# Performance work log

Hardware: AMD Instinct MI355X
Metric: run time of the kernel (lower is better)

Reference implementation:

```python
import jax, jax.numpy as jnp
import numpy as np


def setup_inputs() -> dict:
    key = jax.random.key(0)
    k1, k2 = jax.random.split(key)
    x = jax.random.normal(k1, (2, 320, 4, 32, 32), dtype=jnp.float32)
    W = jax.random.uniform(k2, (640, 1), dtype=jnp.float32)  # torch.rand init
    return {"x": x, "W": W}


def reference(x, W):
    # x: [B, C, D, H, W_], W: [2C, 1]
    B, C, D, H, W_ = x.shape
    N = D * H * W_
    p = x.reshape(B, C, N)  # proj_temp
    w1 = W[:C, 0]   # multiplies temp[k] (the varying row of temp_b)
    w2 = W[C:, 0]   # multiplies temp[j] (the broadcast row)
    s1 = jnp.einsum('bcn,c->bn', p, w1)  # per-position score for column index k
    s2 = jnp.einsum('bcn,c->bn', p, w2)  # per-position score for row index j
    # energy[b, j, k] = w1 . x_k + w2 . x_j  (additive outer-sum decomposition)
    energy = s1[:, None, :] + s2[:, :, None]  # [B, N, N]
    attention = jax.nn.softmax(jax.nn.leaky_relu(energy, negative_slope=0.01), axis=-1)
    # out = bmm(p, attention^T): out[b,c,n] = sum_k p[b,c,k] * attention[b,n,k]
    out = jnp.einsum('bck,bnk->bcn', p, attention) + p
    return out.reshape(B, C, D, H, W_)
```

## Files before the change

### kernel.cpp

```cpp
#include <hip/hip_runtime.h>
#include <hip/hip_bf16.h>

#define C_DIM 320
#define N_DIM 4096
#define NEG 0.01f

typedef float f32x4 __attribute__((ext_vector_type(4)));
typedef float f32x2 __attribute__((ext_vector_type(2)));
typedef short bf16x8 __attribute__((ext_vector_type(8)));
typedef __bf16 bfv8 __attribute__((ext_vector_type(8)));

__device__ __forceinline__ float lrelu(float e) { return fmaxf(e, NEG * e); }

__device__ __forceinline__ unsigned short bf16bits(float v) {
    __hip_bfloat16 h = __float2bfloat16(v);
    return *(unsigned short*)&h;
}
__device__ __forceinline__ float bf16tof(unsigned short u) {
    unsigned int bits = ((unsigned int)u) << 16;
    return __builtin_bit_cast(float, bits);
}

__device__ __forceinline__ void gload_lds16(const void* g, void* l) {
    __builtin_amdgcn_global_load_lds(
        (const __attribute__((address_space(1))) void*)g,
        (__attribute__((address_space(3))) void*)l, 16, 0, 0);
}

__device__ __forceinline__ float fold5(const float* __restrict__ p, int b, int i) {
    float v = p[((size_t)(b * 5 + 0)) * N_DIM + i];
    v += p[((size_t)(b * 5 + 1)) * N_DIM + i];
    v += p[((size_t)(b * 5 + 2)) * N_DIM + i];
    v += p[((size_t)(b * 5 + 3)) * N_DIM + i];
    v += p[((size_t)(b * 5 + 4)) * N_DIM + i];
    return v;
}


__global__ __launch_bounds__(256) void k_pre(const float* __restrict__ x,
                                             const float* __restrict__ W,
                                             float* __restrict__ s1p,
                                             float* __restrict__ s2p,
                                             short* __restrict__ xT) {
    __shared__ float tile[64][65];
    __shared__ float r1[4][64], r2[4][64];
    const int b = blockIdx.z, cg = blockIdx.y, nb = blockIdx.x;
    const int nl = threadIdx.x & 63, cw = threadIdx.x >> 6;
    const int n0 = nb * 64, c0 = cg * 64;
    const int n = n0 + nl;
    float a1 = 0.f, a2 = 0.f;
    #pragma unroll
    for (int cc = 0; cc < 16; ++cc) {
        const int cl = cw * 16 + cc;
        const int c = c0 + cl;
        float v = x[((size_t)(b * C_DIM + c)) * N_DIM + n];
        a1 = fmaf(v, W[c], a1);
        a2 = fmaf(v, W[C_DIM + c], a2);
        tile[cl][nl] = v;
    }
    r1[cw][nl] = a1; r2[cw][nl] = a2;
    __syncthreads();
    const int half = nl >> 5;
    const int cp = nl & 31;
    #pragma unroll
    for (int rr = 0; rr < 8; ++rr) {
        const int nr = cw * 16 + rr * 2 + half;
        unsigned int pk = (unsigned int)bf16bits(tile[2 * cp][nr])
                        | ((unsigned int)bf16bits(tile[2 * cp + 1][nr]) << 16);
        *(unsigned int*)&xT[((size_t)b * N_DIM + n0 + nr) * C_DIM + c0 + 2 * cp] = pk;
    }
    if (threadIdx.x < 64) {
        float t1 = r1[0][nl] + r1[1][nl] + r1[2][nl] + r1[3][nl];
        float t2 = r2[0][nl] + r2[1][nl] + r2[2][nl] + r2[3][nl];
        s1p[((size_t)(b * 5 + cg)) * N_DIM + n] = t1;
        s2p[((size_t)(b * 5 + cg)) * N_DIM + n] = t2;
    }
}

__global__ __launch_bounds__(256) void k_rank(const float* __restrict__ s1p,
                                              int* __restrict__ pcnt) {
    __shared__ float ch[512];
    const int chunk = blockIdx.x, kt = blockIdx.y, b = blockIdx.z;
    const int tid = threadIdx.x;
    const int kbase = chunk * 512;
    ch[tid] = fold5(s1p, b, kbase + tid);
    ch[tid + 256] = fold5(s1p, b, kbase + tid + 256);
    __syncthreads();
    const int k = kt * 256 + tid;
    const float v = fold5(s1p, b, k);
    int cnt = 0;
    #pragma unroll 8
    for (int i = 0; i < 512; ++i) {
        float sv = ch[i];
        int kc = kbase + i;
        cnt += (sv < v || (sv == v && kc < k)) ? 1 : 0;
    }
    pcnt[(b * 8 + chunk) * N_DIM + k] = cnt;
}

__global__ __launch_bounds__(1024) void k_sct(const float* __restrict__ s1p,
                                              const int* __restrict__ pcnt,
                                              float* __restrict__ Sg,
                                              int* __restrict__ idxg,
                                              float* __restrict__ EP,
                                              float* __restrict__ GP,
                                              float* __restrict__ Eg,
                                              float* __restrict__ Gg) {
    __shared__ float sv[4096];
    __shared__ int si[4096];
    __shared__ float wte[16], wtg[16];
    const int b = blockIdx.x, tid = threadIdx.x;
    #pragma unroll
    for (int q = 0; q < 4; ++q) {
        const int k = q * 1024 + tid;
        int r = 0;
        #pragma unroll
        for (int c = 0; c < 8; ++c) r += pcnt[(b * 8 + c) * N_DIM + k];
        sv[r] = fold5(s1p, b, k);
        si[r] = k;
    }
    __syncthreads();
    const int j0 = tid * 4;
    float pe[4], pg[4];
    {
        float v0 = sv[j0], v1 = sv[j0 + 1], v2 = sv[j0 + 2], v3 = sv[j0 + 3];
        float e0 = __expf(v0), e1 = __expf(v1), e2 = __expf(v2), e3 = __expf(v3);
        float g0 = __expf(NEG * v0), g1 = __expf(NEG * v1);
        float g2 = __expf(NEG * v2), g3 = __expf(NEG * v3);
        Eg[b * N_DIM + j0] = e0; Eg[b * N_DIM + j0 + 1] = e1;
        Eg[b * N_DIM + j0 + 2] = e2; Eg[b * N_DIM + j0 + 3] = e3;
        Gg[b * N_DIM + j0] = g0; Gg[b * N_DIM + j0 + 1] = g1;
        Gg[b * N_DIM + j0 + 2] = g2; Gg[b * N_DIM + j0 + 3] = g3;
        pe[0] = e0; pe[1] = pe[0] + e1; pe[2] = pe[1] + e2; pe[3] = pe[2] + e3;
        pg[0] = g0; pg[1] = pg[0] + g1; pg[2] = pg[1] + g2; pg[3] = pg[2] + g3;
    }
    const float te = pe[3], tg = pg[3];
    const int lane = tid & 63, wid = tid >> 6;
    float ie = te, ig = tg;
    #pragma unroll
    for (int o = 1; o < 64; o <<= 1) {
        float ue = __shfl_up(ie, o);
        float ug = __shfl_up(ig, o);
        if (lane >= o) { ie += ue; ig += ug; }
    }
    if (lane == 63) { wte[wid] = ie; wtg[wid] = ig; }
    __syncthreads();
    float oe = 0.f, og = 0.f;
    for (int wq = 0; wq < wid; ++wq) { oe += wte[wq]; og += wtg[wq]; }
    const float be = oe + ie - te, bg = og + ig - tg;
    #pragma unroll
    for (int i = 0; i < 4; ++i) {
        EP[b * 4097 + j0 + i] = be + (i ? pe[i - 1] : 0.f);
        GP[b * 4097 + j0 + i] = bg + (i ? pg[i - 1] : 0.f);
    }
    if (tid == 1023) {
        EP[b * 4097 + 4096] = oe + ie;
        GP[b * 4097 + 4096] = og + ig;
    }
    #pragma unroll
    for (int q = 0; q < 4; ++q) {
        const int j = q * 1024 + tid;
        Sg[b * N_DIM + j] = sv[j];
        idxg[b * N_DIM + j] = si[j];
    }
}

__global__ __launch_bounds__(256) void k_pjz(const short* __restrict__ xT,
                                             const int* __restrict__ idxg,
                                             const float* __restrict__ Eg,
                                             const float* __restrict__ Gg,
                                             const float* __restrict__ Sg,
                                             const float* __restrict__ EP,
                                             const float* __restrict__ GP,
                                             const float* __restrict__ s2p,
                                             unsigned int* __restrict__ Tloc,
                                             float* __restrict__ tot,
                                             int* __restrict__ JnA,
                                             float* __restrict__ fzA,
                                             float* __restrict__ hzA) {
    __shared__ float Sl[4096];
    const int w = threadIdx.x >> 6, l = threadIdx.x & 63;
    const int bx = blockIdx.x;
    if (bx < 160) {
        const int jt4 = bx & 15;
        const int cg = (bx >> 4) % 5;
        const int b = bx / 80;
        const int tile = jt4 * 4 + w;
        const int jbase = tile * 64;
        const int c = cg * 64 + l;
        const short* xTb = xT + (size_t)b * N_DIM * C_DIM;
        const float ej = Eg[b * N_DIM + jbase + l];
        const float gj = Gg[b * N_DIM + jbase + l];
        const int   ij = idxg[b * N_DIM + jbase + l];
        unsigned short xv[64];
        #pragma unroll
        for (int j = 0; j < 64; ++j) {
            const int kidx = __shfl(ij, j);
            xv[j] = (unsigned short)xTb[(size_t)kidx * C_DIM + c];
        }
        float se = 0.f, sg = 0.f;
        #pragma unroll
        for (int j = 0; j < 64; ++j) {
            const float e = __shfl(ej, j);
            const float g = __shfl(gj, j);
            const float x0 = bf16tof(xv[j]);
            se = fmaf(x0, e, se);
            sg = fmaf(x0, g, sg);
            Tloc[((size_t)b * N_DIM + jbase + j) * C_DIM + c] =
                (unsigned int)bf16bits(se) | ((unsigned int)bf16bits(sg) << 16);
        }
        *(f32x2*)&tot[(((size_t)b * 64 + tile) * C_DIM + c) * 2] = (f32x2){se, sg};
    } else {
        const int jb = bx - 160;
        const int b = jb >> 4;
        const int nbase = (jb & 15) * 256;
        for (int i = threadIdx.x; i < 4096; i += 256) Sl[i] = Sg[b * N_DIM + i];
        __syncthreads();
        const float smax = Sl[4095];
        const float EPt = EP[b * 4097 + 4096];
        const int n = nbase + threadIdx.x;
        const float s2n = fold5(s2p, b, n);
        const float mn = lrelu(s2n + smax);
        const float F = __expf(s2n - mn), H = __expf(NEG * s2n - mn);
        const float t = -s2n;
        int lo = 0, hi = 4096;
        while (lo < hi) {
            int mid = (lo + hi) >> 1;
            if (Sl[mid] < t) lo = mid + 1; else hi = mid;
        }
        const float suf = EPt - EP[b * 4097 + lo];
        const float pre = GP[b * 4097 + lo];
        const float rz = 1.f / (F * suf + H * pre);
        JnA[b * N_DIM + n] = lo;
        fzA[b * N_DIM + n] = F * rz;
        hzA[b * N_DIM + n] = H * rz;
    }
}

__global__ __launch_bounds__(256) void k_out(const float* __restrict__ x,
                                             const unsigned int* __restrict__ Tloc,
                                             const float* __restrict__ tot,
                                             const int* __restrict__ JnA,
                                             const float* __restrict__ fzA,
                                             const float* __restrict__ hzA,
                                             float* __restrict__ out) {
    __shared__ float offl[65][64][2];
    __shared__ float wsum[4][64][2];
    __shared__ float tile[64][65];
    const int b = blockIdx.z, cg = blockIdx.y, n0 = blockIdx.x * 64;
    const int tid = threadIdx.x, w = tid >> 6, l = tid & 63;
    const int c0 = cg * 64;

    float ae = 0.f, ag = 0.f;
    #pragma unroll
    for (int i = 0; i < 16; ++i) {
        const int jt = w * 16 + i;
        offl[jt][l][0] = ae; offl[jt][l][1] = ag;
        f32x2 v = *(const f32x2*)&tot[(((size_t)b * 64 + jt) * C_DIM + c0 + l) * 2];
        ae += v[0]; ag += v[1];
    }
    wsum[w][l][0] = ae; wsum[w][l][1] = ag;
    __syncthreads();
    float be = 0.f, bg = 0.f;
    for (int ww = 0; ww < w; ++ww) { be += wsum[ww][l][0]; bg += wsum[ww][l][1]; }
    #pragma unroll
    for (int i = 0; i < 16; ++i) {
        const int jt = w * 16 + i;
        offl[jt][l][0] += be; offl[jt][l][1] += bg;
    }
    if (w == 3) { offl[64][l][0] = be + ae; offl[64][l][1] = bg + ag; }
    __syncthreads();

    const float gtE = offl[64][l][0];

    #pragma unroll
    for (int half = 0; half < 2; ++half) {
        unsigned int tvp[8];
        f32x2 ov[8];
        float fzs[8], hzs[8], msk[8];
        #pragma unroll
        for (int i = 0; i < 8; ++i) {
            const int n = n0 + w * 16 + half * 8 + i;
            const int Jn = JnA[b * N_DIM + n];
            fzs[i] = fzA[b * N_DIM + n];
            hzs[i] = hzA[b * N_DIM + n];
            const int jt = Jn >> 6, jl = Jn & 63;
            msk[i] = jl ? 1.f : 0.f;
            const int jrow = jl ? (Jn - 1) : 0;
            ov[i][0] = offl[jt][l][0];
            ov[i][1] = offl[jt][l][1];
            tvp[i] = Tloc[((size_t)b * N_DIM + jrow) * C_DIM + c0 + l];
        }
        #pragma unroll
        for (int i = 0; i < 8; ++i) {
            const float tvE = bf16tof((unsigned short)(tvp[i] & 0xFFFFu));
            const float tvG = bf16tof((unsigned short)(tvp[i] >> 16));
            const float se_ex = ov[i][0] + msk[i] * tvE;
            const float sg_ex = ov[i][1] + msk[i] * tvG;
            tile[l][w * 16 + half * 8 + i] = fzs[i] * (gtE - se_ex) + hzs[i] * sg_ex;
        }
    }
    __syncthreads();
    const int row = tid >> 2, nseg = (tid & 3) * 16;
    const size_t gidx = ((size_t)(b * C_DIM + c0 + row)) * N_DIM + n0 + nseg;
    #pragma unroll
    for (int i2 = 0; i2 < 16; i2 += 4) {
        f32x4 xv = *(const f32x4*)&x[gidx + i2];
        f32x4 o;
        #pragma unroll
        for (int q = 0; q < 4; ++q) o[q] = tile[row][nseg + i2 + q] + xv[q];
        *(f32x4*)&out[gidx + i2] = o;
    }
}


__global__ __launch_bounds__(256) void k_s12(const float* __restrict__ x,
                                             const float* __restrict__ W,
                                             float* __restrict__ s1p,
                                             float* __restrict__ s2p,
                                             short* __restrict__ xb) {
    const int b = blockIdx.z, cb = blockIdx.y;
    const int nl = threadIdx.x & 63, cw = threadIdx.x >> 6;
    const int n = blockIdx.x * 64 + nl;
    const int cbase = cb * 64 + cw * 16;
    const float* px = x + ((size_t)b * C_DIM + cbase) * N_DIM + n;
    short* pxb = xb + ((size_t)b * C_DIM + cbase) * N_DIM + n;
    const float* w1 = W + cbase;
    const float* w2 = W + C_DIM + cbase;
    float a1 = 0.f, a2 = 0.f;
    #pragma unroll
    for (int cc = 0; cc < 16; ++cc) {
        float v = px[(size_t)cc * N_DIM];
        a1 = fmaf(v, w1[cc], a1);
        a2 = fmaf(v, w2[cc], a2);
        __hip_bfloat16 hv = __float2bfloat16(v);
        pxb[(size_t)cc * N_DIM] = *(short*)&hv;
    }
    __shared__ float r1[4][64], r2[4][64];
    r1[cw][nl] = a1; r2[cw][nl] = a2;
    __syncthreads();
    if (threadIdx.x < 64) {
        s1p[((size_t)b * 5 + cb) * N_DIM + n] = r1[0][nl] + r1[1][nl] + r1[2][nl] + r1[3][nl];
        s2p[((size_t)b * 5 + cb) * N_DIM + n] = r2[0][nl] + r2[1][nl] + r2[2][nl] + r2[3][nl];
    }
}

__global__ __launch_bounds__(1024) void k_fold(const float* __restrict__ s1p,
                                               const float* __restrict__ s2p,
                                               float* __restrict__ s2,
                                               float* __restrict__ Ekf,
                                               float* __restrict__ Gkf,
                                               float* __restrict__ s1max) {
    const int b = blockIdx.x, tid = threadIdx.x;
    __shared__ float md[1024];
    float mx = -3.4e38f;
    for (int n = tid; n < N_DIM; n += 1024) {
        float v1 = 0.f, v2 = 0.f;
        #pragma unroll
        for (int cb = 0; cb < 5; ++cb) {
            v1 += s1p[((size_t)b * 5 + cb) * N_DIM + n];
            v2 += s2p[((size_t)b * 5 + cb) * N_DIM + n];
        }
        s2[b * N_DIM + n] = v2;
        Ekf[b * N_DIM + n] = __expf(v1);
        Gkf[b * N_DIM + n] = __expf(NEG * v1);
        mx = fmaxf(mx, v1);
    }
    md[tid] = mx;
    __syncthreads();
    for (int s = 512; s > 0; s >>= 1) {
        if (tid < s) md[tid] = fmaxf(md[tid], md[tid + s]);
        __syncthreads();
    }
    if (tid == 0) s1max[b] = md[0];
}

__global__ __launch_bounds__(256) void k_z(const float* __restrict__ s2,
                                           const float* __restrict__ s1max,
                                           const float* __restrict__ Ekf,
                                           const float* __restrict__ Gkf,
                                           float* __restrict__ Fz,
                                           float* __restrict__ Hz) {
    __shared__ __align__(16) float Els[4096], Gls[4096];
    const int b = blockIdx.y, tid = threadIdx.x;
    const int w = tid >> 6, l = tid & 63;
    const float* Eb = Ekf + b * N_DIM;
    const float* Gb = Gkf + b * N_DIM;
    #pragma unroll
    for (int i = 0; i < 4; ++i) {
        int chn = i * 256 + tid;
        *(f32x4*)&Els[chn * 4] = *(const f32x4*)&Eb[chn * 4];
        *(f32x4*)&Gls[chn * 4] = *(const f32x4*)&Gb[chn * 4];
    }
    __syncthreads();
    float smax = s1max[b];
    #pragma unroll
    for (int rr = 0; rr < 4; ++rr) {
        int row = b * N_DIM + blockIdx.x * 16 + w * 4 + rr;
        float s2n = s2[row];
        float mn = lrelu(s2n + smax);
        float F = __expf(s2n - mn), H = __expf(NEG * s2n - mn);
        float sum = 0.f;
        #pragma unroll 4
        for (int i = 0; i < 16; ++i) {
            int k = i * 256 + l * 4;
            f32x4 e = *(const f32x4*)&Els[k];
            f32x4 gg = *(const f32x4*)&Gls[k];
            #pragma unroll
            for (int j = 0; j < 4; ++j) sum += fmaxf(e[j] * F, gg[j] * H);
        }
        #pragma unroll
        for (int off = 32; off > 0; off >>= 1) sum += __shfl_down(sum, off);
        if (l == 0) {
            float rz = 1.f / sum;
            Fz[row] = F * rz;
            Hz[row] = H * rz;
        }
    }
}

__global__ __launch_bounds__(128) void k_gemm(const short* __restrict__ xb,
                                              const float* __restrict__ x,
                                              const float* __restrict__ Ekf,
                                              const float* __restrict__ Gkf,
                                              const float* __restrict__ Fz,
                                              const float* __restrict__ Hz,
                                              float* __restrict__ out) {
    __shared__ __align__(16) short Asm[2][2][4096];
    __shared__ __align__(16) float EGs[2][2][256];

    const int b = blockIdx.z, c0 = blockIdx.y * 64, n0 = blockIdx.x * 64;
    const int tid = threadIdx.x;
    const int h = tid >> 6, l = tid & 63, lr = l & 15, g = l >> 4;
    const short* xbp = xb + (size_t)b * C_DIM * N_DIM + h * 2048;
    const float* Eb = Ekf + b * N_DIM + h * 2048;
    const float* Gb = Gkf + b * N_DIM + h * 2048;

    int ncol[4]; float fz[4], hz[4];
    #pragma unroll
    for (int t = 0; t < 4; ++t) {
        int n = n0 + t * 16 + lr;
        ncol[t] = n;
        fz[t] = Fz[b * N_DIM + n];
        hz[t] = Hz[b * N_DIM + n];
    }

    f32x4 acc[4][4];
    #pragma unroll
    for (int i = 0; i < 4; ++i)
        #pragma unroll
        for (int t = 0; t < 4; ++t) acc[i][t] = (f32x4){0.f, 0.f, 0.f, 0.f};

    auto stageA = [&](int buf, int it) {
        #pragma unroll
        for (int i = 0; i < 8; ++i) {
            int row = i * 8 + (l >> 3);
            int c8 = (l & 7) ^ (row & 7);
            gload_lds16(xbp + (size_t)(c0 + row) * N_DIM + it * 64 + c8 * 8,
                        &Asm[h][buf][i * 512]);
        }
    };
    auto stageEG = [&](int buf, int it) {
        int lm = l & 31;
        const float* p = (lm < 16) ? (Eb + it * 64 + lm * 4)
                                   : (Gb + it * 64 + (lm - 16) * 4);
        gload_lds16(p, &EGs[h][buf][0]);
    };

    stageA(0, 0); stageEG(0, 0);
    for (int it = 0; it < 32; ++it) {
        const int buf = it & 1;
        if (it < 31) {
            stageA(buf ^ 1, it + 1);
            stageEG(buf ^ 1, it + 1);
            asm volatile("s_waitcnt vmcnt(9)" ::: "memory");
        } else {
            asm volatile("s_waitcnt vmcnt(0)" ::: "memory");
        }
        __builtin_amdgcn_sched_barrier(0);
        #pragma unroll
        for (int s = 0; s < 2; ++s) {
            const int kk = s * 32 + g * 8;
            f32x4 e0 = *(const f32x4*)&EGs[h][buf][kk];
            f32x4 e1 = *(const f32x4*)&EGs[h][buf][kk + 4];
            f32x4 g0 = *(const f32x4*)&EGs[h][buf][64 + kk];
            f32x4 g1 = *(const f32x4*)&EGs[h][buf][64 + kk + 4];
            bf16x8 afr[4];
            #pragma unroll
            for (int i = 0; i < 4; ++i) {
                int row = 16 * i + lr;
                int idx = row * 64 + (((4 * s + g) ^ (row & 7)) * 8);
                afr[i] = *(const bf16x8*)&Asm[h][buf][idx];
            }
            bf16x8 bfr[4];
            #pragma unroll
            for (int t = 0; t < 4; ++t) {
                bfv8 qv;
                #pragma unroll
                for (int j = 0; j < 4; ++j) {
                    qv[j]     = (__bf16)fmaxf(e0[j] * fz[t], g0[j] * hz[t]);
                    qv[j + 4] = (__bf16)fmaxf(e1[j] * fz[t], g1[j] * hz[t]);
                }
                bfr[t] = __builtin_bit_cast(bf16x8, qv);
            }
            #pragma unroll
            for (int i = 0; i < 4; ++i)
                #pragma unroll
                for (int t = 0; t < 4; ++t)
                    acc[i][t] = __builtin_amdgcn_mfma_f32_16x16x32_bf16(
                        afr[i], bfr[t], acc[i][t], 0, 0, 0);
        }
    }

    __syncthreads();
    float* red = (float*)&Asm[0][0][0];
    if (h == 1) {
        #pragma unroll
        for (int i = 0; i < 4; ++i)
            #pragma unroll
            for (int t = 0; t < 4; ++t)
                #pragma unroll
                for (int r = 0; r < 4; ++r)
                    red[((i * 4 + t) * 4 + r) * 64 + l] = acc[i][t][r];
    }
    __syncthreads();
    if (h == 0) {
        #pragma unroll
        for (int i = 0; i < 4; ++i)
            #pragma unroll
            for (int t = 0; t < 4; ++t)
                #pragma unroll
                for (int r = 0; r < 4; ++r) {
                    float v = acc[i][t][r] + red[((i * 4 + t) * 4 + r) * 64 + l];
                    int c = c0 + 16 * i + g * 4 + r;
                    size_t idx = ((size_t)(b * C_DIM + c)) * N_DIM + ncol[t];
                    out[idx] = v + x[idx];
                }
    }
}


extern "C" void kernel_launch(void* const* d_in, const int* in_sizes, int n_in,
                              void* d_out, int out_size, void* d_ws, size_t ws_size,
                              hipStream_t stream) {
    const float* x = (const float*)d_in[0];
    const float* W = (const float*)d_in[1];
    float* out = (float*)d_out;
    float* ws = (float*)d_ws;

    const size_t o_s1p = 0,
                 o_s2p = 40960,
                 o_S   = 81920,
                 o_idx = 90112,
                 o_Eg  = 98304,
                 o_Gg  = 106496,
                 o_EP  = 114688,
                 o_GP  = 122882,
                 o_Jn  = 131076,
                 o_fz  = 139268,
                 o_hz  = 147460,
                 o_pc  = 155652,
                 o_tot = 221188,
                 o_xT  = 303108,
                 o_Tl  = 1613828,
                 o_end = 4235268;
    const size_t need_new = o_end * 4;

    const size_t m_s1p = 0, m_s2p = 40960, m_s2 = 81920, m_Ek = 90112,
                 m_Gk = 98304, m_Fz = 106496, m_Hz = 114688, m_mx = 122880,
                 m_xb = 122888;
    const size_t need_mid = m_xb * 4 + (size_t)2 * C_DIM * N_DIM * 2;

    if (ws_size >= need_new) {
        float* s1p = ws + o_s1p;
        float* s2p = ws + o_s2p;
        float* Sg = ws + o_S;
        int*   idxg = (int*)(ws + o_idx);
        float* Eg = ws + o_Eg;
        float* Gg = ws + o_Gg;
        float* EP = ws + o_EP;
        float* GP = ws + o_GP;
        int*   JnA = (int*)(ws + o_Jn);
        float* fzA = ws + o_fz;
        float* hzA = ws + o_hz;
        int*   pcnt = (int*)(ws + o_pc);
        float* tot = ws + o_tot;
        short* xT = (short*)(ws + o_xT);
        unsigned int* Tloc = (unsigned int*)(ws + o_Tl);

        k_pre <<<dim3(64, 5, 2), 256, 0, stream>>>(x, W, s1p, s2p, xT);
        k_rank<<<dim3(8, 16, 2), 256, 0, stream>>>(s1p, pcnt);
        k_sct <<<2, 1024, 0, stream>>>(s1p, pcnt, Sg, idxg, EP, GP, Eg, Gg);
        k_pjz <<<192, 256, 0, stream>>>(xT, idxg, Eg, Gg, Sg, EP, GP, s2p,
                                        Tloc, tot, JnA, fzA, hzA);
        k_out <<<dim3(64, 5, 2), 256, 0, stream>>>(x, Tloc, tot, JnA, fzA, hzA, out);
    } else {
        float* s1p = ws + m_s1p;
        float* s2p = ws + m_s2p;
        float* s2  = ws + m_s2;
        float* Ekf = ws + m_Ek;
        float* Gkf = ws + m_Gk;
        float* Fz  = ws + m_Fz;
        float* Hz  = ws + m_Hz;
        float* s1max = ws + m_mx;
        short* xb = (short*)(ws + m_xb);
        k_s12 <<<dim3(64, 5, 2), 256, 0, stream>>>(x, W, s1p, s2p, xb);
        k_fold<<<2, 1024, 0, stream>>>(s1p, s2p, s2, Ekf, Gkf, s1max);
        k_z   <<<dim3(256, 2), 256, 0, stream>>>(s2, s1max, Ekf, Gkf, Fz, Hz);
        k_gemm<<<dim3(64, 5, 2), 128, 0, stream>>>(xb, x, Ekf, Gkf, Fz, Hz, out);
    }
}
```

Before: 48.42 us.

## Parallelize scatter kernel and move prefix scan into z-computation blocks

The scatter kernel, previously two 1024-thread blocks that also computed prefix sums, becomes a 32-block grid. Each thread writes its sorted value, index and exponentials directly to the slot given by its rank. The exclusive prefix sums of E and G are now recomputed inside each of the 32 z-computing blocks of k_pjz, using shared-memory scans. This spreads a serial, two-block step across more CUs and removes the EP/GP global round trip. In exchange the scan work is repeated per block and k_pjz uses more shared memory (about 48 KB).

```diff
diff --git a/kernel.cpp b/kernel.cpp
--- a/kernel.cpp
+++ b/kernel.cpp
@@ -98,71 +98,22 @@
     pcnt[(b * 8 + chunk) * N_DIM + k] = cnt;
 }
 
-__global__ __launch_bounds__(1024) void k_sct(const float* __restrict__ s1p,
-                                              const int* __restrict__ pcnt,
-                                              float* __restrict__ Sg,
-                                              int* __restrict__ idxg,
-                                              float* __restrict__ EP,
-                                              float* __restrict__ GP,
-                                              float* __restrict__ Eg,
-                                              float* __restrict__ Gg) {
-    __shared__ float sv[4096];
-    __shared__ int si[4096];
-    __shared__ float wte[16], wtg[16];
-    const int b = blockIdx.x, tid = threadIdx.x;
-    #pragma unroll
-    for (int q = 0; q < 4; ++q) {
-        const int k = q * 1024 + tid;
-        int r = 0;
-        #pragma unroll
-        for (int c = 0; c < 8; ++c) r += pcnt[(b * 8 + c) * N_DIM + k];
-        sv[r] = fold5(s1p, b, k);
-        si[r] = k;
-    }
-    __syncthreads();
-    const int j0 = tid * 4;
-    float pe[4], pg[4];
-    {
-        float v0 = sv[j0], v1 = sv[j0 + 1], v2 = sv[j0 + 2], v3 = sv[j0 + 3];
-        float e0 = __expf(v0), e1 = __expf(v1), e2 = __expf(v2), e3 = __expf(v3);
-        float g0 = __expf(NEG * v0), g1 = __expf(NEG * v1);
-        float g2 = __expf(NEG * v2), g3 = __expf(NEG * v3);
-        Eg[b * N_DIM + j0] = e0; Eg[b * N_DIM + j0 + 1] = e1;
-        Eg[b * N_DIM + j0 + 2] = e2; Eg[b * N_DIM + j0 + 3] = e3;
-        Gg[b * N_DIM + j0] = g0; Gg[b * N_DIM + j0 + 1] = g1;
-        Gg[b * N_DIM + j0 + 2] = g2; Gg[b * N_DIM + j0 + 3] = g3;
-        pe[0] = e0; pe[1] = pe[0] + e1; pe[2] = pe[1] + e2; pe[3] = pe[2] + e3;
-        pg[0] = g0; pg[1] = pg[0] + g1; pg[2] = pg[1] + g2; pg[3] = pg[2] + g3;
-    }
-    const float te = pe[3], tg = pg[3];
-    const int lane = tid & 63, wid = tid >> 6;
-    float ie = te, ig = tg;
-    #pragma unroll
-    for (int o = 1; o < 64; o <<= 1) {
-        float ue = __shfl_up(ie, o);
-        float ug = __shfl_up(ig, o);
-        if (lane >= o) { ie += ue; ig += ug; }
-    }
-    if (lane == 63) { wte[wid] = ie; wtg[wid] = ig; }
-    __syncthreads();
-    float oe = 0.f, og = 0.f;
-    for (int wq = 0; wq < wid; ++wq) { oe += wte[wq]; og += wtg[wq]; }
-    const float be = oe + ie - te, bg = og + ig - tg;
-    #pragma unroll
-    for (int i = 0; i < 4; ++i) {
-        EP[b * 4097 + j0 + i] = be + (i ? pe[i - 1] : 0.f);
-        GP[b * 4097 + j0 + i] = bg + (i ? pg[i - 1] : 0.f);
-    }
-    if (tid == 1023) {
-        EP[b * 4097 + 4096] = oe + ie;
-        GP[b * 4097 + 4096] = og + ig;
-    }
-    #pragma unroll
-    for (int q = 0; q < 4; ++q) {
-        const int j = q * 1024 + tid;
-        Sg[b * N_DIM + j] = sv[j];
-        idxg[b * N_DIM + j] = si[j];
-    }
+__global__ __launch_bounds__(256) void k_sct(const float* __restrict__ s1p,
+                                             const int* __restrict__ pcnt,
+                                             float* __restrict__ Sg,
+                                             int* __restrict__ idxg,
+                                             float* __restrict__ Eg,
+                                             float* __restrict__ Gg) {
+    const int b = blockIdx.y;
+    const int k = blockIdx.x * 256 + threadIdx.x;
+    int r = 0;
+    #pragma unroll
+    for (int c = 0; c < 8; ++c) r += pcnt[(b * 8 + c) * N_DIM + k];
+    const float v = fold5(s1p, b, k);
+    Sg[b * N_DIM + r] = v;
+    idxg[b * N_DIM + r] = k;
+    Eg[b * N_DIM + r] = __expf(v);
+    Gg[b * N_DIM + r] = __expf(NEG * v);
 }
 
 __global__ __launch_bounds__(256) void k_pjz(const short* __restrict__ xT,
@@ -170,8 +121,6 @@
                                              const float* __restrict__ Eg,
                                              const float* __restrict__ Gg,
                                              const float* __restrict__ Sg,
-                                             const float* __restrict__ EP,
-                                             const float* __restrict__ GP,
                                              const float* __restrict__ s2p,
                                              unsigned int* __restrict__ Tloc,
                                              float* __restrict__ tot,
@@ -179,6 +128,8 @@
                                              float* __restrict__ fzA,
                                              float* __restrict__ hzA) {
     __shared__ float Sl[4096];
+    __shared__ float Ei[4096], Gi[4096];
+    __shared__ float wsE[4], wsG[4];
     const int w = threadIdx.x >> 6, l = threadIdx.x & 63;
     const int bx = blockIdx.x;
     if (bx < 160) {
@@ -214,11 +165,41 @@
         const int jb = bx - 160;
         const int b = jb >> 4;
         const int nbase = (jb & 15) * 256;
-        for (int i = threadIdx.x; i < 4096; i += 256) Sl[i] = Sg[b * N_DIM + i];
+        const int tid = threadIdx.x;
+        for (int i = tid; i < 4096; i += 256) Sl[i] = Sg[b * N_DIM + i];
+        float pe[16], pg[16];
+        float se = 0.f, sgg = 0.f;
+        #pragma unroll
+        for (int q = 0; q < 4; ++q) {
+            f32x4 e4 = *(const f32x4*)&Eg[b * N_DIM + tid * 16 + q * 4];
+            f32x4 g4 = *(const f32x4*)&Gg[b * N_DIM + tid * 16 + q * 4];
+            #pragma unroll
+            for (int j = 0; j < 4; ++j) {
+                se += e4[j];  pe[q * 4 + j] = se;
+                sgg += g4[j]; pg[q * 4 + j] = sgg;
+            }
+        }
+        float ie = se, ig = sgg;
+        #pragma unroll
+        for (int o = 1; o < 64; o <<= 1) {
+            float ue = __shfl_up(ie, o);
+            float ug = __shfl_up(ig, o);
+            if (l >= o) { ie += ue; ig += ug; }
+        }
+        if (l == 63) { wsE[w] = ie; wsG[w] = ig; }
         __syncthreads();
+        float oe = 0.f, og = 0.f;
+        for (int ww = 0; ww < w; ++ww) { oe += wsE[ww]; og += wsG[ww]; }
+        const float baseE = oe + ie - se, baseG = og + ig - sgg;
+        #pragma unroll
+        for (int q = 0; q < 16; ++q) {
+            Ei[tid * 16 + q] = baseE + pe[q];
+            Gi[tid * 16 + q] = baseG + pg[q];
+        }
+        __syncthreads();
+        const float EPt = Ei[4095];
         const float smax = Sl[4095];
-        const float EPt = EP[b * 4097 + 4096];
-        const int n = nbase + threadIdx.x;
+        const int n = nbase + tid;
         const float s2n = fold5(s2p, b, n);
         const float mn = lrelu(s2n + smax);
         const float F = __expf(s2n - mn), H = __expf(NEG * s2n - mn);
@@ -228,9 +209,9 @@
             int mid = (lo + hi) >> 1;
             if (Sl[mid] < t) lo = mid + 1; else hi = mid;
         }
-        const float suf = EPt - EP[b * 4097 + lo];
-        const float pre = GP[b * 4097 + lo];
-        const float rz = 1.f / (F * suf + H * pre);
+        const float EPlo = lo ? Ei[lo - 1] : 0.f;
+        const float GPlo = lo ? Gi[lo - 1] : 0.f;
+        const float rz = 1.f / (F * (EPt - EPlo) + H * GPlo);
         JnA[b * N_DIM + n] = lo;
         fzA[b * N_DIM + n] = F * rz;
         hzA[b * N_DIM + n] = H * rz;
@@ -554,8 +535,6 @@
                  o_idx = 90112,
                  o_Eg  = 98304,
                  o_Gg  = 106496,
-                 o_EP  = 114688,
-                 o_GP  = 122882,
                  o_Jn  = 131076,
                  o_fz  = 139268,
                  o_hz  = 147460,
@@ -578,8 +557,6 @@
         int*   idxg = (int*)(ws + o_idx);
         float* Eg = ws + o_Eg;
         float* Gg = ws + o_Gg;
-        float* EP = ws + o_EP;
-        float* GP = ws + o_GP;
         int*   JnA = (int*)(ws + o_Jn);
         float* fzA = ws + o_fz;
         float* hzA = ws + o_hz;
@@ -590,8 +567,8 @@
 
         k_pre <<<dim3(64, 5, 2), 256, 0, stream>>>(x, W, s1p, s2p, xT);
         k_rank<<<dim3(8, 16, 2), 256, 0, stream>>>(s1p, pcnt);
-        k_sct <<<2, 1024, 0, stream>>>(s1p, pcnt, Sg, idxg, EP, GP, Eg, Gg);
-        k_pjz <<<192, 256, 0, stream>>>(xT, idxg, Eg, Gg, Sg, EP, GP, s2p,
+        k_sct <<<dim3(16, 2), 256, 0, stream>>>(s1p, pcnt, Sg, idxg, Eg, Gg);
+        k_pjz <<<192, 256, 0, stream>>>(xT, idxg, Eg, Gg, Sg, s2p,
                                         Tloc, tot, JnA, fzA, hzA);
         k_out <<<dim3(64, 5, 2), 256, 0, stream>>>(x, Tloc, tot, JnA, fzA, hzA, out);
     } else {
```

New measurement: 47.36 us (median of 2 runs). 2.2% less time.
